# Performance work log

Measured on AMD Instinct MI355X. Metric: run time of the kernel, lower is better.

## Reference

```python
import jax, jax.numpy as jnp
import numpy as np

NH, HD, NKV = 32, 128, 8      # query heads, head dim, kv heads (GQA group = 4)
BS = 16                        # cache block size
NB = 4096                      # number of cache blocks
MB = 128                       # max blocks per sequence (max kv len = 2048)
S = 32                         # decode sequences, 1 new token each
SCALE = 1.0 / float(np.sqrt(HD))
F8 = jnp.float8_e4m3fn


def setup_inputs() -> dict:
    key = jax.random.key(0)
    ks = jax.random.split(key, 10)
    q = jax.random.normal(ks[0], (S, NH * HD), dtype=jnp.float32)
    k = jax.random.normal(ks[1], (S, NKV * HD), dtype=jnp.float32)
    v = jax.random.normal(ks[2], (S, NKV * HD), dtype=jnp.float32)
    k_cache = jax.random.normal(ks[3], (NB, BS, NKV, HD), dtype=jnp.float32)
    v_cache = jax.random.normal(ks[4], (NB, BS, NKV, HD), dtype=jnp.float32)
    k_scale = jax.random.uniform(ks[5], (NKV,), minval=0.5, maxval=1.5, dtype=jnp.float32)
    v_scale = jax.random.uniform(ks[6], (NKV,), minval=0.5, maxval=1.5, dtype=jnp.float32)
    # unique blocks per sequence: permutation of all NB blocks (NB == S*MB)
    block_tables = jax.random.permutation(ks[7], NB).reshape(S, MB).astype(jnp.int64)
    context_lens = jax.random.randint(ks[8], (S,), 64, MB * BS + 1).astype(jnp.int64)
    # slot of the newly generated token: position context_len-1 inside its block table
    last = context_lens - 1
    blk = jnp.take_along_axis(block_tables, (last // BS)[:, None], axis=1)[:, 0]
    slot_mapping = (blk * BS + last % BS).astype(jnp.int64)
    return {"q": q, "k": k, "v": v, "k_cache": k_cache, "v_cache": v_cache,
            "k_scale": k_scale, "v_scale": v_scale, "slot_mapping": slot_mapping,
            "block_tables": block_tables, "context_lens": context_lens}


def reference(q, k, v, k_cache, v_cache, k_scale, v_scale, slot_mapping, block_tables, context_lens):
    s = q.shape[0]
    G = NH // NKV
    qr = q.reshape(s, NKV, G, HD)              # [S, nkvh, g, hd]
    kn = k.reshape(s, NKV, HD)                 # [S, nkvh, hd]
    vn = v.reshape(s, NKV, HD)
    # --- store_kvcache: quantize new K/V to fp8 with per-kv-head scale, scatter at slot_mapping
    kq = (kn / k_scale[None, :, None]).astype(F8).astype(jnp.float32)
    vq = (vn / v_scale[None, :, None]).astype(F8).astype(jnp.float32)
    kc = k_cache.reshape(NB * BS, NKV, HD).at[slot_mapping].set(kq)
    vc = v_cache.reshape(NB * BS, NKV, HD).at[slot_mapping].set(vq)
    # --- FP8 dequant of cache (view-as-fp8, * scale, -> bf16), as in unified 'static' decode
    kd = (kc.astype(F8).astype(jnp.float32) * k_scale[None, :, None]).astype(jnp.bfloat16)
    vd = (vc.astype(F8).astype(jnp.float32) * v_scale[None, :, None]).astype(jnp.bfloat16)
    # --- paged gather via block tables -> per-seq contiguous KV of length L = MB*BS
    slots = (block_tables[:, :, None] * BS + jnp.arange(BS)[None, None, :]).reshape(s, MB * BS)
    Kg = kd[slots]                              # [S, L, nkvh, hd]
    Vg = vd[slots]
    L = MB * BS
    ctx = jnp.maximum(context_lens, 1)
    # --- GQA decode attention (1 query token per sequence)
    scores = jnp.einsum('shgd,slhd->shgl', qr.astype(jnp.float32), Kg.astype(jnp.float32)) * SCALE
    mask = jnp.arange(L)[None, :] < ctx[:, None]            # [S, L]
    scores = jnp.where(mask[:, None, None, :], scores, -jnp.inf)
    p = jax.nn.softmax(scores, axis=-1)
    o = jnp.einsum('shgl,slhd->shgd', p, Vg.astype(jnp.float32))
    return o.reshape(s, NH * HD)
```

## Files before the change

### kernel.cpp

```cpp
#include <hip/hip_runtime.h>
#include <hip/hip_bf16.h>

#define NH   32
#define HD   128
#define NKV  8
#define GQ   4
#define BS   16
#define NB   4096
#define MB   128
#define SEQ  32
#define WPG  8
#define UPW  8
#define NSPLIT (WPG*UPW)
#define UNROLL 4

__constant__ float SCALE_RSQRT = 0.08838834764831845f;

typedef float v2f __attribute__((ext_vector_type(2)));

__device__ __forceinline__ float bf16r(float x) {
  unsigned u = __float_as_uint(x);
  u = (u + 0x7fffu + ((u >> 16) & 1u)) & 0xffff0000u;
  return __uint_as_float(u);
}

__device__ __forceinline__ float4 deq4(float4 x, float sc) {
  int p0 = __builtin_amdgcn_cvt_pk_fp8_f32(x.x, x.y, 0, false);
  int p1 = __builtin_amdgcn_cvt_pk_fp8_f32(x.z, x.w, 0, false);
  v2f a = __builtin_amdgcn_cvt_pk_f32_fp8(p0, false);
  v2f b = __builtin_amdgcn_cvt_pk_f32_fp8(p1, false);
  float4 r;
  r.x = bf16r(a.x * sc);
  r.y = bf16r(a.y * sc);
  r.z = bf16r(b.x * sc);
  r.w = bf16r(b.y * sc);
  return r;
}

__global__ __launch_bounds__(256, 4)
void attn_split(const float* __restrict__ q,
                const float* __restrict__ knew,
                const float* __restrict__ vnew,
                const float* __restrict__ k_cache,
                const float* __restrict__ v_cache,
                const float* __restrict__ k_scale,
                const float* __restrict__ v_scale,
                const int* __restrict__ block_tables,
                const int* __restrict__ context_lens,
                float* __restrict__ o_part,
                float2* __restrict__ ml_part) {
  const int wg = blockIdx.x;
  const int wgsub = wg % WPG;
  const int h = (wg / WPG) % NKV;
  const int s = wg / (WPG * NKV);
  const int tid = threadIdx.x;
  const int lane = tid & 31;
  const int unit = tid >> 5;
  const int ug = wgsub * UPW + unit;
  const int dbase = lane * 4;

  __shared__ int bt[MB];
  __shared__ float so[UPW][GQ][HD];
  __shared__ float2 sml[UPW][GQ];

  if (tid < MB) bt[tid] = block_tables[s * MB + tid];
  __syncthreads();

  const int ctx = context_lens[s];
  const int last = ctx - 1;
  const float ks = k_scale[h];
  const float vs = v_scale[h];

  float4 qv[GQ];
#pragma unroll
  for (int g = 0; g < GQ; ++g) {
    float4 t = *(const float4*)(q + ((size_t)s * NH + h * GQ + g) * HD + dbase);
    qv[g].x = t.x * SCALE_RSQRT;
    qv[g].y = t.y * SCALE_RSQRT;
    qv[g].z = t.z * SCALE_RSQRT;
    qv[g].w = t.w * SCALE_RSQRT;
  }

  float m[GQ], l[GQ];
  float4 oacc[GQ];
#pragma unroll
  for (int g = 0; g < GQ; ++g) {
    m[g] = -1e30f;
    l[g] = 0.0f;
    oacc[g] = make_float4(0.f, 0.f, 0.f, 0.f);
  }

  if (ug == (last & (NSPLIT - 1))) {
    float4 kk = *(const float4*)(knew + ((size_t)s * NKV + h) * HD + dbase);
    float4 vt = *(const float4*)(vnew + ((size_t)s * NKV + h) * HD + dbase);
    kk.x /= ks; kk.y /= ks; kk.z /= ks; kk.w /= ks;
    vt.x /= vs; vt.y /= vs; vt.z /= vs; vt.w /= vs;
    kk = deq4(kk, ks);
    vt = deq4(vt, vs);
#pragma unroll
    for (int g = 0; g < GQ; ++g) {
      float d = kk.x * qv[g].x + kk.y * qv[g].y + kk.z * qv[g].z + kk.w * qv[g].w;
      d += __shfl_xor(d, 1);
      d += __shfl_xor(d, 2);
      d += __shfl_xor(d, 4);
      d += __shfl_xor(d, 8);
      d += __shfl_xor(d, 16);
      m[g] = d;
      l[g] = 1.0f;
      oacc[g] = vt;
    }
  }

  for (int t0 = ug; t0 < ctx; t0 += NSPLIT * UNROLL) {
    float4 kk[UNROLL], vv[UNROLL];
    bool val[UNROLL];
#pragma unroll
    for (int i = 0; i < UNROLL; ++i) {
      int t = t0 + i * NSPLIT;
      val[i] = (t < ctx) && (t != last);
      kk[i] = make_float4(0.f, 0.f, 0.f, 0.f);
      vv[i] = make_float4(0.f, 0.f, 0.f, 0.f);
      if (val[i]) {
        int blk = bt[t >> 4];
        size_t off = (((size_t)blk * BS + (t & (BS - 1))) * NKV + h) * HD + dbase;
        kk[i] = *(const float4*)(k_cache + off);
        vv[i] = *(const float4*)(v_cache + off);
      }
    }

    float sc[UNROLL][GQ];
#pragma unroll
    for (int i = 0; i < UNROLL; ++i) {
      float4 kd = deq4(kk[i], ks);
      vv[i] = deq4(vv[i], vs);
#pragma unroll
      for (int g = 0; g < GQ; ++g) {
        float d = kd.x * qv[g].x + kd.y * qv[g].y + kd.z * qv[g].z + kd.w * qv[g].w;
        d += __shfl_xor(d, 1);
        d += __shfl_xor(d, 2);
        d += __shfl_xor(d, 4);
        d += __shfl_xor(d, 8);
        d += __shfl_xor(d, 16);
        sc[i][g] = val[i] ? d : -1e30f;
      }
    }

#pragma unroll
    for (int g = 0; g < GQ; ++g) {
      float tm = sc[0][g];
#pragma unroll
      for (int i = 1; i < UNROLL; ++i) tm = fmaxf(tm, sc[i][g]);
      float mnew = fmaxf(m[g], tm);
      float alpha = __expf(m[g] - mnew);
      float p[UNROLL];
      float lad = 0.f;
#pragma unroll
      for (int i = 0; i < UNROLL; ++i) {
        p[i] = __expf(sc[i][g] - mnew);
        lad += p[i];
      }
      l[g] = l[g] * alpha + lad;
      float4 acc = make_float4(0.f, 0.f, 0.f, 0.f);
#pragma unroll
      for (int i = 0; i < UNROLL; ++i) {
        acc.x += p[i] * vv[i].x;
        acc.y += p[i] * vv[i].y;
        acc.z += p[i] * vv[i].z;
        acc.w += p[i] * vv[i].w;
      }
      oacc[g].x = oacc[g].x * alpha + acc.x;
      oacc[g].y = oacc[g].y * alpha + acc.y;
      oacc[g].z = oacc[g].z * alpha + acc.z;
      oacc[g].w = oacc[g].w * alpha + acc.w;
      m[g] = mnew;
    }
  }

#pragma unroll
  for (int g = 0; g < GQ; ++g)
    *(float4*)&so[unit][g][dbase] = oacc[g];
  if (lane == 0) {
#pragma unroll
    for (int g = 0; g < GQ; ++g) sml[unit][g] = make_float2(m[g], l[g]);
  }
  __syncthreads();

  if (tid < 128) {
    int g = tid >> 5;
    int ln = tid & 31;
    float M = -1e30f;
#pragma unroll
    for (int u = 0; u < UPW; ++u) M = fmaxf(M, sml[u][g].x);
    float L = 0.f;
    float4 acc = make_float4(0.f, 0.f, 0.f, 0.f);
#pragma unroll
    for (int u = 0; u < UPW; ++u) {
      float w = __expf(sml[u][g].x - M);
      L += sml[u][g].y * w;
      float4 t = *(const float4*)&so[u][g][ln * 4];
      acc.x += w * t.x;
      acc.y += w * t.y;
      acc.z += w * t.z;
      acc.w += w * t.w;
    }
    size_t ob = ((((size_t)s * NKV + h) * WPG + wgsub) * GQ + g) * HD + ln * 4;
    *(float4*)(o_part + ob) = acc;
    if (ln == 0)
      ml_part[(((size_t)s * NKV + h) * WPG + wgsub) * GQ + g] = make_float2(M, L);
  }
}

__global__ void combine_splits(const float* __restrict__ o_part,
                               const float2* __restrict__ ml_part,
                               float* __restrict__ out) {
  int b = blockIdx.x;
  int h = b % NKV;
  int s = b / NKV;
  int d = threadIdx.x;
#pragma unroll
  for (int g = 0; g < GQ; ++g) {
    float2 ml[WPG];
    float M = -1e30f;
#pragma unroll
    for (int i = 0; i < WPG; ++i) {
      ml[i] = ml_part[(((size_t)s * NKV + h) * WPG + i) * GQ + g];
      M = fmaxf(M, ml[i].x);
    }
    float L = 0.f;
    float acc = 0.f;
#pragma unroll
    for (int i = 0; i < WPG; ++i) {
      float w = __expf(ml[i].x - M);
      L += ml[i].y * w;
      acc += w * o_part[((((size_t)s * NKV + h) * WPG + i) * GQ + g) * HD + d];
    }
    out[((size_t)s * NH + h * GQ + g) * HD + d] = acc / L;
  }
}

extern "C" void kernel_launch(void* const* d_in, const int* in_sizes, int n_in,
                              void* d_out, int out_size, void* d_ws, size_t ws_size,
                              hipStream_t stream) {
  const float* q        = (const float*)d_in[0];
  const float* k        = (const float*)d_in[1];
  const float* v        = (const float*)d_in[2];
  const float* k_cache  = (const float*)d_in[3];
  const float* v_cache  = (const float*)d_in[4];
  const float* k_scale  = (const float*)d_in[5];
  const float* v_scale  = (const float*)d_in[6];
  const int*   btables  = (const int*)d_in[8];
  const int*   ctx_lens = (const int*)d_in[9];
  float*       out      = (float*)d_out;

  float*  o_part  = (float*)d_ws;
  float2* ml_part = (float2*)((char*)d_ws +
                     (size_t)SEQ * NKV * WPG * GQ * HD * sizeof(float));

  attn_split<<<SEQ * NKV * WPG, 256, 0, stream>>>(
      q, k, v, k_cache, v_cache, k_scale, v_scale, btables, ctx_lens,
      o_part, ml_part);

  combine_splits<<<SEQ * NKV, 128, 0, stream>>>(o_part, ml_part, out);
}
```

Before: 486.9 us.

## Map kv heads to warps within a workgroup and drop in-block split reduction

```diff
diff --git a/kernel.cpp b/kernel.cpp
--- a/kernel.cpp
+++ b/kernel.cpp
@@ -9,9 +9,7 @@
 #define NB   4096
 #define MB   128
 #define SEQ  32
-#define WPG  8
-#define UPW  8
-#define NSPLIT (WPG*UPW)
+#define J    64
 #define UNROLL 4
 
 __constant__ float SCALE_RSQRT = 0.08838834764831845f;
@@ -50,26 +48,14 @@
                 float* __restrict__ o_part,
                 float2* __restrict__ ml_part) {
   const int wg = blockIdx.x;
-  const int wgsub = wg % WPG;
-  const int h = (wg / WPG) % NKV;
-  const int s = wg / (WPG * NKV);
+  const int wgsub = wg % J;
+  const int s = wg / J;
   const int tid = threadIdx.x;
   const int lane = tid & 31;
-  const int unit = tid >> 5;
-  const int ug = wgsub * UPW + unit;
+  const int h = tid >> 5;
   const int dbase = lane * 4;
 
   __shared__ int bt[MB];
-  __shared__ float so[UPW][GQ][HD];
-  __shared__ float2 sml[UPW][GQ];
-
-  if (tid < MB) bt[tid] = block_tables[s * MB + tid];
-  __syncthreads();
-
-  const int ctx = context_lens[s];
-  const int last = ctx - 1;
-  const float ks = k_scale[h];
-  const float vs = v_scale[h];
 
   float4 qv[GQ];
 #pragma unroll
@@ -81,6 +67,14 @@
     qv[g].w = t.w * SCALE_RSQRT;
   }
 
+  if (tid < MB) bt[tid] = block_tables[s * MB + tid];
+  __syncthreads();
+
+  const int ctx = context_lens[s];
+  const int last = ctx - 1;
+  const float ks = k_scale[h];
+  const float vs = v_scale[h];
+
   float m[GQ], l[GQ];
   float4 oacc[GQ];
 #pragma unroll
@@ -90,7 +84,7 @@
     oacc[g] = make_float4(0.f, 0.f, 0.f, 0.f);
   }
 
-  if (ug == (last & (NSPLIT - 1))) {
+  if (wgsub == (last & (J - 1))) {
     float4 kk = *(const float4*)(knew + ((size_t)s * NKV + h) * HD + dbase);
     float4 vt = *(const float4*)(vnew + ((size_t)s * NKV + h) * HD + dbase);
     kk.x /= ks; kk.y /= ks; kk.z /= ks; kk.w /= ks;
@@ -111,12 +105,12 @@
     }
   }
 
-  for (int t0 = ug; t0 < ctx; t0 += NSPLIT * UNROLL) {
+  for (int t0 = wgsub; t0 < ctx; t0 += J * UNROLL) {
     float4 kk[UNROLL], vv[UNROLL];
     bool val[UNROLL];
 #pragma unroll
     for (int i = 0; i < UNROLL; ++i) {
-      int t = t0 + i * NSPLIT;
+      int t = t0 + i * J;
       val[i] = (t < ctx) && (t != last);
       kk[i] = make_float4(0.f, 0.f, 0.f, 0.f);
       vv[i] = make_float4(0.f, 0.f, 0.f, 0.f);
@@ -176,66 +170,40 @@
     }
   }
 
+  const size_t pb = (((size_t)s * NKV + h) * J + wgsub) * GQ;
 #pragma unroll
   for (int g = 0; g < GQ; ++g)
-    *(float4*)&so[unit][g][dbase] = oacc[g];
+    *(float4*)(o_part + (pb + g) * HD + dbase) = oacc[g];
   if (lane == 0) {
 #pragma unroll
-    for (int g = 0; g < GQ; ++g) sml[unit][g] = make_float2(m[g], l[g]);
-  }
-  __syncthreads();
-
-  if (tid < 128) {
-    int g = tid >> 5;
-    int ln = tid & 31;
-    float M = -1e30f;
-#pragma unroll
-    for (int u = 0; u < UPW; ++u) M = fmaxf(M, sml[u][g].x);
-    float L = 0.f;
-    float4 acc = make_float4(0.f, 0.f, 0.f, 0.f);
-#pragma unroll
-    for (int u = 0; u < UPW; ++u) {
-      float w = __expf(sml[u][g].x - M);
-      L += sml[u][g].y * w;
-      float4 t = *(const float4*)&so[u][g][ln * 4];
-      acc.x += w * t.x;
-      acc.y += w * t.y;
-      acc.z += w * t.z;
-      acc.w += w * t.w;
-    }
-    size_t ob = ((((size_t)s * NKV + h) * WPG + wgsub) * GQ + g) * HD + ln * 4;
-    *(float4*)(o_part + ob) = acc;
-    if (ln == 0)
-      ml_part[(((size_t)s * NKV + h) * WPG + wgsub) * GQ + g] = make_float2(M, L);
+    for (int g = 0; g < GQ; ++g)
+      ml_part[pb + g] = make_float2(m[g], l[g]);
   }
 }
 
 __global__ void combine_splits(const float* __restrict__ o_part,
                                const float2* __restrict__ ml_part,
                                float* __restrict__ out) {
-  int b = blockIdx.x;
-  int h = b % NKV;
-  int s = b / NKV;
-  int d = threadIdx.x;
-#pragma unroll
-  for (int g = 0; g < GQ; ++g) {
-    float2 ml[WPG];
-    float M = -1e30f;
-#pragma unroll
-    for (int i = 0; i < WPG; ++i) {
-      ml[i] = ml_part[(((size_t)s * NKV + h) * WPG + i) * GQ + g];
-      M = fmaxf(M, ml[i].x);
-    }
-    float L = 0.f;
-    float acc = 0.f;
-#pragma unroll
-    for (int i = 0; i < WPG; ++i) {
-      float w = __expf(ml[i].x - M);
-      L += ml[i].y * w;
-      acc += w * o_part[((((size_t)s * NKV + h) * WPG + i) * GQ + g) * HD + d];
-    }
-    out[((size_t)s * NH + h * GQ + g) * HD + d] = acc / L;
-  }
+  const int b = blockIdx.x;
+  const int g = b % GQ;
+  const int sh = b / GQ;
+  const int h = sh % NKV;
+  const int s = sh / NKV;
+  const int d = threadIdx.x;
+  const size_t mlbase = (size_t)sh * J * GQ + g;
+
+  float M = -1e30f;
+  for (int i = 0; i < J; ++i)
+    M = fmaxf(M, ml_part[mlbase + (size_t)i * GQ].x);
+
+  float L = 0.f, acc = 0.f;
+  for (int i = 0; i < J; ++i) {
+    float2 t = ml_part[mlbase + (size_t)i * GQ];
+    float w = __expf(t.x - M);
+    L += t.y * w;
+    acc += w * o_part[(mlbase + (size_t)i * GQ) * HD + d];
+  }
+  out[((size_t)s * NH + h * GQ + g) * HD + d] = acc / L;
 }
 
 extern "C" void kernel_launch(void* const* d_in, const int* in_sizes, int n_in,
@@ -254,11 +222,11 @@
 
   float*  o_part  = (float*)d_ws;
   float2* ml_part = (float2*)((char*)d_ws +
-                     (size_t)SEQ * NKV * WPG * GQ * HD * sizeof(float));
-
-  attn_split<<<SEQ * NKV * WPG, 256, 0, stream>>>(
+                     (size_t)SEQ * NKV * J * GQ * HD * sizeof(float));
+
+  attn_split<<<SEQ * J, 256, 0, stream>>>(
       q, k, v, k_cache, v_cache, k_scale, v_scale, btables, ctx_lens,
       o_part, ml_part);
 
-  combine_splits<<<SEQ * NKV, 128, 0, stream>>>(o_part, ml_part, out);
-}
+  combine_splits<<<SEQ * NKV * GQ, 128, 0, stream>>>(o_part, ml_part, out);
+}
```

Measured after the change: 503.6 us. 3.4% more time.

## Fuse split-KV attention and combine into one workgroup per sequence-head

Applied to the files above, without the earlier changes.

```diff
diff --git a/kernel.cpp b/kernel.cpp
--- a/kernel.cpp
+++ b/kernel.cpp
@@ -9,9 +9,7 @@
 #define NB   4096
 #define MB   128
 #define SEQ  32
-#define WPG  8
-#define UPW  8
-#define NSPLIT (WPG*UPW)
+#define UNITS 16
 #define UNROLL 4
 
 __constant__ float SCALE_RSQRT = 0.08838834764831845f;
@@ -37,8 +35,8 @@
   return r;
 }
 
-__global__ __launch_bounds__(256, 4)
-void attn_split(const float* __restrict__ q,
+__global__ __launch_bounds__(512, 2)
+void attn_fused(const float* __restrict__ q,
                 const float* __restrict__ knew,
                 const float* __restrict__ vnew,
                 const float* __restrict__ k_cache,
@@ -47,29 +45,18 @@
                 const float* __restrict__ v_scale,
                 const int* __restrict__ block_tables,
                 const int* __restrict__ context_lens,
-                float* __restrict__ o_part,
-                float2* __restrict__ ml_part) {
+                float* __restrict__ out) {
   const int wg = blockIdx.x;
-  const int wgsub = wg % WPG;
-  const int h = (wg / WPG) % NKV;
-  const int s = wg / (WPG * NKV);
+  const int h = wg % NKV;
+  const int s = wg / NKV;
   const int tid = threadIdx.x;
   const int lane = tid & 31;
   const int unit = tid >> 5;
-  const int ug = wgsub * UPW + unit;
   const int dbase = lane * 4;
 
   __shared__ int bt[MB];
-  __shared__ float so[UPW][GQ][HD];
-  __shared__ float2 sml[UPW][GQ];
-
-  if (tid < MB) bt[tid] = block_tables[s * MB + tid];
-  __syncthreads();
-
-  const int ctx = context_lens[s];
-  const int last = ctx - 1;
-  const float ks = k_scale[h];
-  const float vs = v_scale[h];
+  __shared__ float so[UNITS][GQ][HD];
+  __shared__ float2 sml[UNITS][GQ];
 
   float4 qv[GQ];
 #pragma unroll
@@ -81,6 +68,14 @@
     qv[g].w = t.w * SCALE_RSQRT;
   }
 
+  if (tid < MB) bt[tid] = block_tables[s * MB + tid];
+  __syncthreads();
+
+  const int ctx = context_lens[s];
+  const int last = ctx - 1;
+  const float ks = k_scale[h];
+  const float vs = v_scale[h];
+
   float m[GQ], l[GQ];
   float4 oacc[GQ];
 #pragma unroll
@@ -90,7 +85,7 @@
     oacc[g] = make_float4(0.f, 0.f, 0.f, 0.f);
   }
 
-  if (ug == (last & (NSPLIT - 1))) {
+  if (unit == (last & (UNITS - 1))) {
     float4 kk = *(const float4*)(knew + ((size_t)s * NKV + h) * HD + dbase);
     float4 vt = *(const float4*)(vnew + ((size_t)s * NKV + h) * HD + dbase);
     kk.x /= ks; kk.y /= ks; kk.z /= ks; kk.w /= ks;
@@ -111,12 +106,12 @@
     }
   }
 
-  for (int t0 = ug; t0 < ctx; t0 += NSPLIT * UNROLL) {
+  for (int t0 = unit; t0 < ctx; t0 += UNITS * UNROLL) {
     float4 kk[UNROLL], vv[UNROLL];
     bool val[UNROLL];
 #pragma unroll
     for (int i = 0; i < UNROLL; ++i) {
-      int t = t0 + i * NSPLIT;
+      int t = t0 + i * UNITS;
       val[i] = (t < ctx) && (t != last);
       kk[i] = make_float4(0.f, 0.f, 0.f, 0.f);
       vv[i] = make_float4(0.f, 0.f, 0.f, 0.f);
@@ -190,11 +185,11 @@
     int ln = tid & 31;
     float M = -1e30f;
 #pragma unroll
-    for (int u = 0; u < UPW; ++u) M = fmaxf(M, sml[u][g].x);
+    for (int u = 0; u < UNITS; ++u) M = fmaxf(M, sml[u][g].x);
     float L = 0.f;
     float4 acc = make_float4(0.f, 0.f, 0.f, 0.f);
 #pragma unroll
-    for (int u = 0; u < UPW; ++u) {
+    for (int u = 0; u < UNITS; ++u) {
       float w = __expf(sml[u][g].x - M);
       L += sml[u][g].y * w;
       float4 t = *(const float4*)&so[u][g][ln * 4];
@@ -203,38 +198,9 @@
       acc.z += w * t.z;
       acc.w += w * t.w;
     }
-    size_t ob = ((((size_t)s * NKV + h) * WPG + wgsub) * GQ + g) * HD + ln * 4;
-    *(float4*)(o_part + ob) = acc;
-    if (ln == 0)
-      ml_part[(((size_t)s * NKV + h) * WPG + wgsub) * GQ + g] = make_float2(M, L);
-  }
-}
-
-__global__ void combine_splits(const float* __restrict__ o_part,
-                               const float2* __restrict__ ml_part,
-                               float* __restrict__ out) {
-  int b = blockIdx.x;
-  int h = b % NKV;
-  int s = b / NKV;
-  int d = threadIdx.x;
-#pragma unroll
-  for (int g = 0; g < GQ; ++g) {
-    float2 ml[WPG];
-    float M = -1e30f;
-#pragma unroll
-    for (int i = 0; i < WPG; ++i) {
-      ml[i] = ml_part[(((size_t)s * NKV + h) * WPG + i) * GQ + g];
-      M = fmaxf(M, ml[i].x);
-    }
-    float L = 0.f;
-    float acc = 0.f;
-#pragma unroll
-    for (int i = 0; i < WPG; ++i) {
-      float w = __expf(ml[i].x - M);
-      L += ml[i].y * w;
-      acc += w * o_part[((((size_t)s * NKV + h) * WPG + i) * GQ + g) * HD + d];
-    }
-    out[((size_t)s * NH + h * GQ + g) * HD + d] = acc / L;
+    float rL = 1.0f / L;
+    acc.x *= rL; acc.y *= rL; acc.z *= rL; acc.w *= rL;
+    *(float4*)(out + ((size_t)s * NH + h * GQ + g) * HD + ln * 4) = acc;
   }
 }
 
@@ -252,13 +218,8 @@
   const int*   ctx_lens = (const int*)d_in[9];
   float*       out      = (float*)d_out;
 
-  float*  o_part  = (float*)d_ws;
-  float2* ml_part = (float2*)((char*)d_ws +
-                     (size_t)SEQ * NKV * WPG * GQ * HD * sizeof(float));
-
-  attn_split<<<SEQ * NKV * WPG, 256, 0, stream>>>(
-      q, k, v, k_cache, v_cache, k_scale, v_scale, btables, ctx_lens,
-      o_part, ml_part);
-
-  combine_splits<<<SEQ * NKV, 128, 0, stream>>>(o_part, ml_part, out);
-}
+  (void)d_ws; (void)ws_size;
+
+  attn_fused<<<SEQ * NKV, 512, 0, stream>>>(
+      q, k, v, k_cache, v_cache, k_scale, v_scale, btables, ctx_lens, out);
+}
```

Result: slower. 501.2 us (+2.9%).
